# Performance work log

Hardware: AMD Instinct MI355X
Metric: run time of the kernel (lower is better)

The kernel has to match this reference:

```python
import jax, jax.numpy as jnp
import numpy as np

L, B, T, I, H, P, O = 2, 64, 512, 512, 512, 256, 512


def setup_inputs() -> dict:
    key = jax.random.key(0)
    ks = iter(jax.random.split(key, 40))
    SCALE = 0.03  # keep gate pre-activations in a sane range

    def w(shape):
        return jax.random.normal(next(ks), shape, jnp.float32) * SCALE

    return {
        "x": jax.random.normal(next(ks), (B, T, I), jnp.float32),
        "Wr": w((L, H, I + H)), "br": jnp.zeros((L, H), jnp.float32),
        "Wu": w((L, H, I + H)), "bu": jnp.ones((L, H), jnp.float32),  # update_gate bias init to 1.0
        "Wn": w((L, H, I + H)), "bn": jnp.zeros((L, H), jnp.float32),
        "Wmr": w((L, P, H)), "bmr": jnp.zeros((L, P), jnp.float32),
        "Wmw": w((L, P, H)), "bmw": jnp.zeros((L, P), jnp.float32),
        "Wmu": w((L, P, H)), "bmu": jnp.zeros((L, P), jnp.float32),
        "Wmh": w((L, H, P)), "bmh": jnp.zeros((L, H), jnp.float32),
        "Wd": w((L, P, H)), "bd": jnp.zeros((L, P), jnp.float32),
        "Ws": w((L, P, H)), "bs": jnp.zeros((L, P), jnp.float32),
        "Wout": w((O, H)), "bout": jnp.zeros((O,), jnp.float32),
        "dopamine": jnp.full((1,), 0.5, jnp.float32),
        "serotonin": jnp.full((1,), 0.5, jnp.float32),
    }


def _lin(x, W, b):
    # x: [B, in], W: [out, in] (torch Linear layout), b: [out]
    return jnp.einsum("bi,oi->bo", x, W) + b


def reference(x, Wr, br, Wu, bu, Wn, bn, Wmr, bmr, Wmw, bmw, Wmu, bmu,
              Wmh, bmh, Wd, bd, Ws, bs, Wout, bout, dopamine, serotonin):
    num_layers = Wr.shape[0]
    bsz = x.shape[0]
    hdim = Wr.shape[1]
    pdim = Wmr.shape[1]
    h0 = jnp.zeros((num_layers, bsz, hdim), x.dtype)
    m0 = jnp.zeros((num_layers, bsz, pdim), x.dtype)

    def step(carry, x_t):
        hidden, memory = carry  # [L,B,H], [L,B,P]
        inp = x_t
        new_h, new_m = [], []
        for l in range(num_layers):
            h, m = hidden[l], memory[l]
            comb = jnp.concatenate([inp, h], axis=-1)
            reset = jax.nn.sigmoid(_lin(comb, Wr[l], br[l]))
            update = jax.nn.sigmoid(_lin(comb, Wu[l], bu[l]))
            comb_r = jnp.concatenate([inp, reset * h], axis=-1)
            new_hid = jnp.tanh(_lin(comb_r, Wn[l], bn[l]))
            h_cand = (1.0 - update) * h + update * new_hid
            read_gate = jax.nn.sigmoid(_lin(h_cand, Wmr[l], bmr[l]))
            mem_out = read_gate * m
            h_mem = h_cand + _lin(mem_out, Wmh[l], bmh[l])
            write_gate = jax.nn.sigmoid(_lin(h_mem, Wmw[l], bmw[l]))
            new_mem_content = jnp.tanh(_lin(h_mem, Wmu[l], bmu[l]))
            dopa = jax.nn.sigmoid(_lin(h_mem, Wd[l], bd[l]) * dopamine)
            write_gate = write_gate * dopa
            sero = jax.nn.sigmoid(_lin(h_mem, Ws[l], bs[l]) * serotonin)
            write_gate = write_gate * (1.0 - sero)
            m_new = (1.0 - write_gate) * m + write_gate * new_mem_content
            inp = h_mem
            new_h.append(h_mem)
            new_m.append(m_new)
        out_t = _lin(inp, Wout, bout)  # [B, O]
        return (jnp.stack(new_h), jnp.stack(new_m)), out_t

    (h_final, m_final), outs = jax.lax.scan(step, (h0, m0), jnp.swapaxes(x, 0, 1))
    outputs = jnp.swapaxes(outs, 0, 1)  # [B, T, O]
    return outputs, h_final, m_final
```

## Files before the change

### kernel.cpp

```cpp
#include <hip/hip_runtime.h>
#include <math.h>

#define BB 64
#define TT 512
#define II 512
#define HH 512
#define PP 256
#define OO 512

#define NBLK 512
#define NTHR 512
#define RPB 4
#define AGT __HIP_MEMORY_SCOPE_AGENT

__device__ __align__(256) double g_h0d[2*BB*HH];
__device__ __align__(256) double g_h1 [BB*HH];
__device__ __align__(256) double g_rh [2*BB*HH];
__device__ __align__(256) double g_hc [2*BB*HH];
__device__ __align__(256) double g_mo [2*BB*PP];
__device__ __align__(256) double g_hist[(long)BB*TT*HH];
__device__ unsigned g_sync[4096];

__device__ __align__(256) float g_WRU [2*1024*1024];
__device__ __align__(256) float g_WnT2[2*512*1024];
__device__ __align__(256) float g_WMG [2*512*1024];
__device__ __align__(256) float g_WmrT[2*512*256];
__device__ __align__(256) float g_WmhT[2*256*512];
__device__ __align__(256) float g_WoutT[512*512];

struct KP {
  const float *x,*Wr,*br,*Wu,*bu,*Wn,*bn,*Wmr,*bmr,*Wmw,*bmw,*Wmu,*bmu,
              *Wmh,*bmh,*Wd,*bd,*Ws,*bs,*Wout,*bout,*dop,*ser;
  float* out;
};

__device__ inline double sigd(double x){ return 1.0/(1.0+exp(-x)); }

__global__ void __launch_bounds__(256) prep(KP p)
{
  __shared__ float tile[32][33];
  const int b = blockIdx.x;
  const int T_RUN = 3072;
  const int T_MG  = T_RUN + 1024;
  const int T_MR  = T_MG  + 256;
  const int T_MH  = T_MR  + 256;
  const int T_OUT = T_MH  + 256;
  const int tid = threadIdx.x;

  const float* src=nullptr; float* dst=nullptr;
  int K=0,C=0,st=1,off=0,k0=0,c0=0,mode=0;
  bool xpose=true;

  if (b < T_RUN){
    int m=b>>10, r=b&1023, l=r>>9, t=r&511;
    K=1024; C=512; int ct=t&15, kt=t>>4; k0=kt*32; c0=ct*32;
    src = (m==0? p.Wr : m==1? p.Wu : p.Wn) + (long)l*C*K;
    if (m<2){ dst = g_WRU + (long)l*1024*1024; st=2; off=m; }
    else    { dst = g_WnT2 + (long)l*512*1024; mode=1; }
  } else if (b < T_MG){
    int q=b-T_RUN, m=q>>8, r=q&255, l=r>>7, t=r&127;
    K=512; C=256; int ct=t&7, kt=t>>3; k0=kt*32; c0=ct*32;
    const float* s4[4]={p.Wmw,p.Wmu,p.Wd,p.Ws};
    src = s4[m] + (long)l*C*K;
    dst = g_WMG + (long)l*512*1024; st=4; off=m;
  } else if (b < T_MR){
    int r=b-T_MG, l=r>>7, t=r&127;
    K=512; C=256; int ct=t&7, kt=t>>3; k0=kt*32; c0=ct*32;
    src = p.Wmr + (long)l*C*K;
    dst = g_WmrT + (long)l*512*256; st=1; off=0;
  } else if (b < T_MH){
    int r=b-T_MR, l=r>>7, t=r&127;
    K=256; C=512; int ct=t&15, kt=t>>4; k0=kt*32; c0=ct*32;
    src = p.Wmh + (long)l*C*K;
    dst = g_WmhT + (long)l*256*512; st=1; off=0;
  } else if (b < T_OUT){
    int t=b-T_MH;
    K=512; C=512; int ct=t&15, kt=t>>4; k0=kt*32; c0=ct*32;
    src = p.Wout; dst = g_WoutT; st=1; off=0;
  } else {
    xpose=false;
    long i = (long)(b-T_OUT)*256 + tid;
    if (i < 2L*BB*HH) g_h0d[i]=0.0;
    if (i < (long)BB*HH) g_h1[i]=0.0;
    if (i < 4096) g_sync[(int)i]=0u;
  }

  if (xpose){
    for (int i=tid;i<1024;i+=256){
      int ty=i>>5, tx=i&31;
      tile[ty][tx] = src[(long)(c0+ty)*K + k0+tx];
    }
    __syncthreads();
    for (int i=tid;i<1024;i+=256){
      int ky=i>>5, cx=i&31;
      int k=k0+ky, c=c0+cx;
      long o = mode ? ((long)(k>>1)*1024 + (long)c*2 + (k&1))
                    : ((long)k*C*st + (long)c*st + off);
      dst[o] = tile[cx][ky];
    }
  }
}

__global__ void __launch_bounds__(NTHR,4) rnn_kernel(KP p)
{
  const int tid=threadIdx.x;
  const int xcd=blockIdx.x&7, lay=xcd>>2, xl=xcd&3;
  const int cs=(blockIdx.x>>3)&3, rb=blockIdx.x>>5;
  const int iw=tid>>6, lane=tid&63;
  const int r0g=rb*RPB;
  const int colH0=xl*128+cs*32, colP0=xl*64+cs*16;
  const int cW = colH0 + iw*4;
  const int pW = colP0 + iw*2;

  __shared__ double sP[RPB][528];
  __shared__ double sH[RPB][528];
  __shared__ double sB[RPB][528];
  __shared__ double sM[RPB][264];
  __shared__ double su[RPB][32];
  __shared__ double sm[RPB][16];

  if (tid<64) sm[tid>>4][tid&15]=0.0;

  auto fs=[](int k){ return k + ((k>>6)<<1); };

  const float* WRU = g_WRU  + (long)lay*1024*1024;
  const float* WN2 = g_WnT2 + (long)lay*512*1024;
  const float* WMGp= g_WMG  + (long)lay*512*1024;
  const float* WMR = g_WmrT + (long)lay*512*256;
  const float* WMH = g_WmhT + (long)lay*256*512;
  const float* br_ = p.br + lay*HH; const float* bu_ = p.bu + lay*HH;
  const float* bn_ = p.bn + lay*HH; const float* bmh_= p.bmh+ lay*HH;
  const float* bmr_= p.bmr+ lay*PP; const float* bmw_= p.bmw+ lay*PP;
  const float* bmu_= p.bmu+ lay*PP; const float* bd_ = p.bd + lay*PP;
  const float* bs_ = p.bs + lay*PP;
  const double dopa = (double)p.dop[0];
  const double sero = (double)p.ser[0];

  double* rhG = g_rh + (long)lay*BB*HH + (long)r0g*HH;
  double* hcG = g_hc + (long)lay*BB*HH + (long)r0g*HH;
  double* moG = g_mo + (long)lay*BB*PP + (long)r0g*PP;

  const int gidx = rb*2 + lay;
  auto bar=[&](int s){
    __syncthreads();
    if (tid==0){
      unsigned* cnt=&g_sync[(gidx*4+s)*32];
      unsigned* gen=cnt+16;
      unsigned ge=__hip_atomic_load(gen,__ATOMIC_RELAXED,AGT);
      unsigned old=__hip_atomic_fetch_add(cnt,1u,__ATOMIC_RELEASE,AGT);
      if (old==15u){
        __hip_atomic_store(cnt,0u,__ATOMIC_RELAXED,AGT);
        __hip_atomic_fetch_add(gen,1u,__ATOMIC_RELEASE,AGT);
      } else {
        while(__hip_atomic_load(gen,__ATOMIC_RELAXED,AGT)==ge) __builtin_amdgcn_s_sleep(1);
      }
      asm volatile("" ::: "memory");
    }
    __syncthreads();
  };
  auto wait_ge=[&](int l,int s,unsigned v){
    if (tid==0){
      unsigned* gen=&g_sync[((rb*2+l)*4+s)*32+16];
      while(__hip_atomic_load(gen,__ATOMIC_RELAXED,AGT)<v) __builtin_amdgcn_s_sleep(1);
      asm volatile("" ::: "memory");
    }
    __syncthreads();
  };

  auto ld512=[&](double dst[RPB][528], const double* src){
    double v[4];
    #pragma unroll
    for (int j=0;j<4;++j){
      int idx=j*512+tid;
      v[j]=__hip_atomic_load(src + (long)(idx>>9)*HH + (idx&511), __ATOMIC_RELAXED, AGT);
    }
    #pragma unroll
    for (int j=0;j<4;++j){
      int idx=j*512+tid; int c=idx&511;
      dst[idx>>9][c + ((c>>6)<<1)] = v[j];
    }
  };
  auto ld256=[&](const double* src){
    double v[2];
    #pragma unroll
    for (int j=0;j<2;++j){
      int idx=j*512+tid;
      v[j]=__hip_atomic_load(src + (long)(idx>>8)*PP + (idx&255), __ATOMIC_RELAXED, AGT);
    }
    #pragma unroll
    for (int j=0;j<2;++j){
      int idx=j*512+tid; int c=idx&255;
      sM[idx>>8][c + ((c>>6)<<1)] = v[j];
    }
  };
  auto ldX=[&](int t){
    float v[4];
    #pragma unroll
    for (int j=0;j<4;++j){
      int idx=j*512+tid;
      v[j]=p.x[((long)(r0g+(idx>>9))*TT + t)*II + (idx&511)];
    }
    #pragma unroll
    for (int j=0;j<4;++j){
      int idx=j*512+tid; int c=idx&511;
      sP[idx>>9][c + ((c>>6)<<1)] = (double)v[j];
    }
  };

  auto ruS=[&](){
    const int c=lane&3, ks=lane>>2;
    const int col=cW+c;
    const float* w = WRU + (long)(ks*64)*1024 + col*2;
    const double* a = (ks<8)? &sP[0][66*ks] : &sH[0][66*(ks-8)];
    double ar[4]={0,0,0,0}, au[4]={0,0,0,0};
    #pragma unroll 4
    for (int k=0;k<64;k+=2){
      float2 w0=*(const float2*)(w + (long)k*1024);
      float2 w1=*(const float2*)(w + (long)(k+1)*1024);
      double wr0=(double)w0.x, wu0=(double)w0.y;
      double wr1=(double)w1.x, wu1=(double)w1.y;
      #pragma unroll
      for (int j=0;j<4;++j){
        double2 av=*(const double2*)(a + j*528 + k);
        ar[j]=fma(av.x,wr0,ar[j]); au[j]=fma(av.x,wu0,au[j]);
        ar[j]=fma(av.y,wr1,ar[j]); au[j]=fma(av.y,wu1,au[j]);
      }
    }
    #pragma unroll
    for (int j=0;j<4;++j){
      ar[j]+=__shfl_xor(ar[j],4);  au[j]+=__shfl_xor(au[j],4);
      ar[j]+=__shfl_xor(ar[j],8);  au[j]+=__shfl_xor(au[j],8);
      ar[j]+=__shfl_xor(ar[j],16); au[j]+=__shfl_xor(au[j],16);
      ar[j]+=__shfl_xor(ar[j],32); au[j]+=__shfl_xor(au[j],32);
    }
    if (lane<4){
      #pragma unroll
      for (int j=0;j<4;++j){
        double r=sigd(ar[j]+(double)br_[col]);
        double u=sigd(au[j]+(double)bu_[col]);
        su[j][iw*4+c]=u;
        __hip_atomic_store(&rhG[(long)j*HH+col], r*sH[j][fs(col)], __ATOMIC_RELAXED, AGT);
      }
    }
  };
  auto nS=[&](){
    const int c=lane&3, ks=lane>>2;
    const int col=cW+c;
    const float* w = WN2 + (long)(ks*32)*1024 + col*2;
    const double* a = (ks<8)? &sP[0][66*ks] : &sB[0][66*(ks-8)];
    double ac[4]={0,0,0,0};
    #pragma unroll 4
    for (int kp=0;kp<32;++kp){
      float2 wv=*(const float2*)(w + (long)kp*1024);
      double w0=(double)wv.x, w1=(double)wv.y;
      #pragma unroll
      for (int j=0;j<4;++j){
        double2 av=*(const double2*)(a + j*528 + kp*2);
        ac[j]=fma(av.x,w0,ac[j]); ac[j]=fma(av.y,w1,ac[j]);
      }
    }
    #pragma unroll
    for (int j=0;j<4;++j){
      ac[j]+=__shfl_xor(ac[j],4);  ac[j]+=__shfl_xor(ac[j],8);
      ac[j]+=__shfl_xor(ac[j],16); ac[j]+=__shfl_xor(ac[j],32);
    }
    if (lane<4){
      #pragma unroll
      for (int j=0;j<4;++j){
        double nh=tanh(ac[j]+(double)bn_[col]);
        double u=su[j][iw*4+c];
        __hip_atomic_store(&hcG[(long)j*HH+col],
          (1.0-u)*sH[j][fs(col)]+u*nh, __ATOMIC_RELAXED, AGT);
      }
    }
  };
  auto mgS=[&](){
    const int pc=lane&1, j=(lane>>1)&3, ks=lane>>3;
    const int pcol=pW+pc;
    const float* w4 = WMGp + (long)(ks*64)*1024 + pcol*4;
    const double* a = &sH[j][66*ks];
    double q0=0,q1=0,q2=0,q3=0;
    #pragma unroll 4
    for (int k=0;k<64;++k){
      double av=a[k];
      float4 v=*(const float4*)(w4 + (long)k*1024);
      q0=fma(av,(double)v.x,q0); q1=fma(av,(double)v.y,q1);
      q2=fma(av,(double)v.z,q2); q3=fma(av,(double)v.w,q3);
    }
    q0+=__shfl_xor(q0,8); q0+=__shfl_xor(q0,16); q0+=__shfl_xor(q0,32);
    q1+=__shfl_xor(q1,8); q1+=__shfl_xor(q1,16); q1+=__shfl_xor(q1,32);
    q2+=__shfl_xor(q2,8); q2+=__shfl_xor(q2,16); q2+=__shfl_xor(q2,32);
    q3+=__shfl_xor(q3,8); q3+=__shfl_xor(q3,16); q3+=__shfl_xor(q3,32);
    if (lane<8){
      double wg=sigd(q0+(double)bmw_[pcol]);
      double nm=tanh(q1+(double)bmu_[pcol]);
      double dp=sigd((q2+(double)bd_[pcol])*dopa);
      double sr=sigd((q3+(double)bs_[pcol])*sero);
      double ww=wg*dp*(1.0-sr);
      sm[j][iw*2+pc]=(1.0-ww)*sm[j][iw*2+pc]+ww*nm;
    }
  };
  auto rgS=[&](){
    const int pc=lane&1, j=(lane>>1)&3, ks=lane>>3;
    const int pcol=pW+pc;
    const float* w = WMR + (long)(ks*64)*256 + pcol;
    const double* a = &sB[j][66*ks];
    double o=0,o2=0;
    #pragma unroll 8
    for (int k=0;k<64;k+=2){
      o =fma(a[k],  (double)w[(long)k*256],    o);
      o2=fma(a[k+1],(double)w[(long)(k+1)*256],o2);
    }
    o+=o2; o+=__shfl_xor(o,8); o+=__shfl_xor(o,16); o+=__shfl_xor(o,32);
    if (lane<8){
      __hip_atomic_store(&moG[(long)j*PP+pcol],
        sigd(o+(double)bmr_[pcol])*sm[j][iw*2+pc], __ATOMIC_RELAXED, AGT);
    }
  };
  auto hmS=[&](int t){
    const int c=lane&3, j=(lane>>2)&3, ks=lane>>4;
    const int col=cW+c;
    const float* w = WMH + (long)(ks*64)*512 + col;
    const double* a = &sM[j][66*ks];
    double o=0,o2=0;
    #pragma unroll 8
    for (int k=0;k<64;k+=2){
      o =fma(a[k],  (double)w[(long)k*512],    o);
      o2=fma(a[k+1],(double)w[(long)(k+1)*512],o2);
    }
    o+=o2; o+=__shfl_xor(o,16); o+=__shfl_xor(o,32);
    if (lane<16){
      double hv = o + (double)bmh_[col] + sB[j][fs(col)];
      long gi=(long)(r0g+j)*HH+col;
      if (lay==0){
        __hip_atomic_store(&g_h0d[(long)(t&1)*BB*HH+gi],hv,__ATOMIC_RELAXED,AGT);
      } else {
        __hip_atomic_store(&g_h1[gi],hv,__ATOMIC_RELAXED,AGT);
        __builtin_nontemporal_store(hv,&g_hist[((long)(r0g+j)*TT+t)*HH+col]);
      }
    }
  };

  for (int t=0; t<TT; ++t){
    if (lay==0){
      ldX(t);
      ld512(sH, &g_h0d[(long)((t+1)&1)*BB*HH + (long)r0g*HH]);
    } else {
      wait_ge(0,3,(unsigned)(t+1));
      ld512(sP, &g_h0d[(long)(t&1)*BB*HH + (long)r0g*HH]);
      ld512(sH, g_h1 + (long)r0g*HH);
    }
    __syncthreads();
    ruS();
    if (t>0) mgS();
    bar(0);
    ld512(sB, rhG);
    __syncthreads();
    nS();
    bar(1);
    ld512(sB, hcG);
    __syncthreads();
    rgS();
    bar(2);
    ld256(moG);
    __syncthreads();
    if (lay==0 && t>=2) wait_ge(1,0,(unsigned)(t-1));
    hmS(t);
    bar(3);
  }

  if (lay==0) ld512(sH, &g_h0d[(long)((TT-1)&1)*BB*HH + (long)r0g*HH]);
  else        ld512(sH, g_h1 + (long)r0g*HH);
  __syncthreads();
  mgS();
  __syncthreads();

  const long ob=(long)BB*TT*OO;
  if (tid<128){
    int r=tid>>5, c=tid&31; int col=colH0+c; long bq=r0g+r;
    p.out[ob + (long)lay*BB*HH + bq*HH + col] = (float)sH[r][fs(col)];
  }
  if (tid<64){
    int r=tid>>4, pc=tid&15; int pcol=colP0+pc; long bq=r0g+r;
    p.out[ob + 2L*BB*HH + (long)lay*BB*PP + bq*PP + pcol] = (float)sm[r][pc];
  }
}

__global__ void __launch_bounds__(512) out_gemm(const float* bout, float* out)
{
  __shared__ double sH[8][512];
  const int tid = threadIdx.x;
  const int iw = tid >> 6, lane = tid & 63;
  const int kq = lane >> 5, c32 = lane & 31;
  const int col = iw*64 + c32*2;
  const float* w = g_WoutT + kq*(256*512) + col;
  for (int rbx = blockIdx.x; rbx < BB*TT/8; rbx += gridDim.x){
    __syncthreads();
    for (int i = tid; i < 8*256; i += 512){
      int rr = i >> 8, c2 = (i & 255) << 1;
      *(double2*)&sH[rr][c2] = *(const double2*)(g_hist + (long)(rbx*8+rr)*HH + c2);
    }
    __syncthreads();
    double s[8][2];
    #pragma unroll
    for (int r=0;r<8;++r){ s[r][0]=0.0; s[r][1]=0.0; }
    #pragma unroll 2
    for (int k=0;k<256;++k){
      float2 wv = *(const float2*)(w + (long)k*512);
      double wx = (double)wv.x, wy = (double)wv.y;
      #pragma unroll
      for (int r=0;r<8;++r){
        double av = sH[r][kq*256 + k];
        s[r][0] = fma(av, wx, s[r][0]);
        s[r][1] = fma(av, wy, s[r][1]);
      }
    }
    #pragma unroll
    for (int r=0;r<8;++r){
      double t0 = s[r][0] + __shfl_xor(s[r][0],32);
      double t1 = s[r][1] + __shfl_xor(s[r][1],32);
      if (lane < 32){
        float2 fv;
        fv.x = (float)(t0 + (double)bout[col]);
        fv.y = (float)(t1 + (double)bout[col+1]);
        *(float2*)&out[(long)(rbx*8+r)*OO + col] = fv;
      }
    }
  }
}

extern "C" void kernel_launch(void* const* d_in, const int* in_sizes, int n_in,
                              void* d_out, int out_size, void* d_ws, size_t ws_size,
                              hipStream_t stream)
{
  KP p;
  p.x   = (const float*)d_in[0];
  p.Wr  = (const float*)d_in[1];  p.br  = (const float*)d_in[2];
  p.Wu  = (const float*)d_in[3];  p.bu  = (const float*)d_in[4];
  p.Wn  = (const float*)d_in[5];  p.bn  = (const float*)d_in[6];
  p.Wmr = (const float*)d_in[7];  p.bmr = (const float*)d_in[8];
  p.Wmw = (const float*)d_in[9];  p.bmw = (const float*)d_in[10];
  p.Wmu = (const float*)d_in[11]; p.bmu = (const float*)d_in[12];
  p.Wmh = (const float*)d_in[13]; p.bmh = (const float*)d_in[14];
  p.Wd  = (const float*)d_in[15]; p.bd  = (const float*)d_in[16];
  p.Ws  = (const float*)d_in[17]; p.bs  = (const float*)d_in[18];
  p.Wout= (const float*)d_in[19]; p.bout= (const float*)d_in[20];
  p.dop = (const float*)d_in[21]; p.ser = (const float*)d_in[22];
  p.out = (float*)d_out;

  prep<<<dim3(5120), dim3(256), 0, stream>>>(p);
  rnn_kernel<<<dim3(NBLK), dim3(NTHR), 0, stream>>>(p);
  out_gemm<<<dim3(2048), dim3(512), 0, stream>>>(p.bout, p.out);
}
```

Before: 69.75 ms.

## Process eight batch rows per block with 1024 threads and half the blocks

```diff
diff --git a/kernel.cpp b/kernel.cpp
--- a/kernel.cpp
+++ b/kernel.cpp
@@ -8,9 +8,9 @@
 #define PP 256
 #define OO 512
 
-#define NBLK 512
-#define NTHR 512
-#define RPB 4
+#define NBLK 256
+#define NTHR 1024
+#define RPB 8
 #define AGT __HIP_MEMORY_SCOPE_AGENT
 
 __device__ __align__(256) double g_h0d[2*BB*HH];
@@ -109,17 +109,19 @@
   const int iw=tid>>6, lane=tid&63;
   const int r0g=rb*RPB;
   const int colH0=xl*128+cs*32, colP0=xl*64+cs*16;
-  const int cW = colH0 + iw*4;
-  const int pW = colP0 + iw*2;
+  const int cW  = colH0 + (iw>>1)*4;
+  const int rset= (iw&1)*4;
+  const int cW2 = colH0 + iw*2;
+  const int pW  = colP0 + iw;
 
   __shared__ double sP[RPB][528];
   __shared__ double sH[RPB][528];
   __shared__ double sB[RPB][528];
-  __shared__ double sM[RPB][264];
+  __shared__ double sM[RPB][265];
   __shared__ double su[RPB][32];
   __shared__ double sm[RPB][16];
 
-  if (tid<64) sm[tid>>4][tid&15]=0.0;
+  if (tid<128) sm[tid>>4][tid&15]=0.0;
 
   auto fs=[](int k){ return k + ((k>>6)<<1); };
 
@@ -171,12 +173,12 @@
     double v[4];
     #pragma unroll
     for (int j=0;j<4;++j){
-      int idx=j*512+tid;
+      int idx=j*1024+tid;
       v[j]=__hip_atomic_load(src + (long)(idx>>9)*HH + (idx&511), __ATOMIC_RELAXED, AGT);
     }
     #pragma unroll
     for (int j=0;j<4;++j){
-      int idx=j*512+tid; int c=idx&511;
+      int idx=j*1024+tid; int c=idx&511;
       dst[idx>>9][c + ((c>>6)<<1)] = v[j];
     }
   };
@@ -184,12 +186,12 @@
     double v[2];
     #pragma unroll
     for (int j=0;j<2;++j){
-      int idx=j*512+tid;
+      int idx=j*1024+tid;
       v[j]=__hip_atomic_load(src + (long)(idx>>8)*PP + (idx&255), __ATOMIC_RELAXED, AGT);
     }
     #pragma unroll
     for (int j=0;j<2;++j){
-      int idx=j*512+tid; int c=idx&255;
+      int idx=j*1024+tid; int c=idx&255;
       sM[idx>>8][c + ((c>>6)<<1)] = v[j];
     }
   };
@@ -197,12 +199,12 @@
     float v[4];
     #pragma unroll
     for (int j=0;j<4;++j){
-      int idx=j*512+tid;
+      int idx=j*1024+tid;
       v[j]=p.x[((long)(r0g+(idx>>9))*TT + t)*II + (idx&511)];
     }
     #pragma unroll
     for (int j=0;j<4;++j){
-      int idx=j*512+tid; int c=idx&511;
+      int idx=j*1024+tid; int c=idx&511;
       sP[idx>>9][c + ((c>>6)<<1)] = (double)v[j];
     }
   };
@@ -211,7 +213,7 @@
     const int c=lane&3, ks=lane>>2;
     const int col=cW+c;
     const float* w = WRU + (long)(ks*64)*1024 + col*2;
-    const double* a = (ks<8)? &sP[0][66*ks] : &sH[0][66*(ks-8)];
+    const double* a = (ks<8)? &sP[rset][66*ks] : &sH[rset][66*(ks-8)];
     double ar[4]={0,0,0,0}, au[4]={0,0,0,0};
     #pragma unroll 4
     for (int k=0;k<64;k+=2){
@@ -234,12 +236,13 @@
       ar[j]+=__shfl_xor(ar[j],32); au[j]+=__shfl_xor(au[j],32);
     }
     if (lane<4){
+      const int colw=cW+lane;
       #pragma unroll
       for (int j=0;j<4;++j){
-        double r=sigd(ar[j]+(double)br_[col]);
-        double u=sigd(au[j]+(double)bu_[col]);
-        su[j][iw*4+c]=u;
-        __hip_atomic_store(&rhG[(long)j*HH+col], r*sH[j][fs(col)], __ATOMIC_RELAXED, AGT);
+        double r=sigd(ar[j]+(double)br_[colw]);
+        double u=sigd(au[j]+(double)bu_[colw]);
+        su[rset+j][(iw>>1)*4+lane]=u;
+        __hip_atomic_store(&rhG[(long)(rset+j)*HH+colw], r*sH[rset+j][fs(colw)], __ATOMIC_RELAXED, AGT);
       }
     }
   };
@@ -247,7 +250,7 @@
     const int c=lane&3, ks=lane>>2;
     const int col=cW+c;
     const float* w = WN2 + (long)(ks*32)*1024 + col*2;
-    const double* a = (ks<8)? &sP[0][66*ks] : &sB[0][66*(ks-8)];
+    const double* a = (ks<8)? &sP[rset][66*ks] : &sB[rset][66*(ks-8)];
     double ac[4]={0,0,0,0};
     #pragma unroll 4
     for (int kp=0;kp<32;++kp){
@@ -265,19 +268,19 @@
       ac[j]+=__shfl_xor(ac[j],16); ac[j]+=__shfl_xor(ac[j],32);
     }
     if (lane<4){
+      const int colw=cW+lane;
       #pragma unroll
       for (int j=0;j<4;++j){
-        double nh=tanh(ac[j]+(double)bn_[col]);
-        double u=su[j][iw*4+c];
-        __hip_atomic_store(&hcG[(long)j*HH+col],
-          (1.0-u)*sH[j][fs(col)]+u*nh, __ATOMIC_RELAXED, AGT);
+        double nh=tanh(ac[j]+(double)bn_[colw]);
+        double u=su[rset+j][(iw>>1)*4+lane];
+        __hip_atomic_store(&hcG[(long)(rset+j)*HH+colw],
+          (1.0-u)*sH[rset+j][fs(colw)]+u*nh, __ATOMIC_RELAXED, AGT);
       }
     }
   };
   auto mgS=[&](){
-    const int pc=lane&1, j=(lane>>1)&3, ks=lane>>3;
-    const int pcol=pW+pc;
-    const float* w4 = WMGp + (long)(ks*64)*1024 + pcol*4;
+    const int j=lane&7, ks=lane>>3;
+    const float* w4 = WMGp + (long)(ks*64)*1024 + pW*4;
     const double* a = &sH[j][66*ks];
     double q0=0,q1=0,q2=0,q3=0;
     #pragma unroll 4
@@ -292,18 +295,17 @@
     q2+=__shfl_xor(q2,8); q2+=__shfl_xor(q2,16); q2+=__shfl_xor(q2,32);
     q3+=__shfl_xor(q3,8); q3+=__shfl_xor(q3,16); q3+=__shfl_xor(q3,32);
     if (lane<8){
-      double wg=sigd(q0+(double)bmw_[pcol]);
-      double nm=tanh(q1+(double)bmu_[pcol]);
-      double dp=sigd((q2+(double)bd_[pcol])*dopa);
-      double sr=sigd((q3+(double)bs_[pcol])*sero);
+      double wg=sigd(q0+(double)bmw_[pW]);
+      double nm=tanh(q1+(double)bmu_[pW]);
+      double dp=sigd((q2+(double)bd_[pW])*dopa);
+      double sr=sigd((q3+(double)bs_[pW])*sero);
       double ww=wg*dp*(1.0-sr);
-      sm[j][iw*2+pc]=(1.0-ww)*sm[j][iw*2+pc]+ww*nm;
+      sm[lane][iw]=(1.0-ww)*sm[lane][iw]+ww*nm;
     }
   };
   auto rgS=[&](){
-    const int pc=lane&1, j=(lane>>1)&3, ks=lane>>3;
-    const int pcol=pW+pc;
-    const float* w = WMR + (long)(ks*64)*256 + pcol;
+    const int j=lane&7, ks=lane>>3;
+    const float* w = WMR + (long)(ks*64)*256 + pW;
     const double* a = &sB[j][66*ks];
     double o=0,o2=0;
     #pragma unroll 8
@@ -313,13 +315,13 @@
     }
     o+=o2; o+=__shfl_xor(o,8); o+=__shfl_xor(o,16); o+=__shfl_xor(o,32);
     if (lane<8){
-      __hip_atomic_store(&moG[(long)j*PP+pcol],
-        sigd(o+(double)bmr_[pcol])*sm[j][iw*2+pc], __ATOMIC_RELAXED, AGT);
+      __hip_atomic_store(&moG[(long)lane*PP+pW],
+        sigd(o+(double)bmr_[pW])*sm[lane][iw], __ATOMIC_RELAXED, AGT);
     }
   };
   auto hmS=[&](int t){
-    const int c=lane&3, j=(lane>>2)&3, ks=lane>>4;
-    const int col=cW+c;
+    const int c=lane&1, j=(lane>>1)&7, ks=lane>>4;
+    const int col=cW2+c;
     const float* w = WMH + (long)(ks*64)*512 + col;
     const double* a = &sM[j][66*ks];
     double o=0,o2=0;
@@ -376,11 +378,11 @@
   __syncthreads();
 
   const long ob=(long)BB*TT*OO;
-  if (tid<128){
+  if (tid<256){
     int r=tid>>5, c=tid&31; int col=colH0+c; long bq=r0g+r;
     p.out[ob + (long)lay*BB*HH + bq*HH + col] = (float)sH[r][fs(col)];
   }
-  if (tid<64){
+  if (tid<128){
     int r=tid>>4, pc=tid&15; int pcol=colP0+pc; long bq=r0g+r;
     p.out[ob + 2L*BB*HH + (long)lay*BB*PP + bq*PP + pcol] = (float)sm[r][pc];
   }
```

New measurement: 67.16 ms. 1.04x faster.
